# Kernel optimization log

Hardware: AMD Instinct MI355X
Metric: run time of the kernel (lower is better)

## Reference

```python
import math
import jax, jax.numpy as jnp
import numpy as np

B, N, C, H = 8, 512, 1024, 16
HD = C // H


def setup_inputs() -> dict:
    key = jax.random.key(0)
    ks = jax.random.split(key, 10)
    s = 0.02
    return {
        "x": jax.random.normal(ks[0], (B, N, C), jnp.float32),
        "mu": jax.random.normal(ks[1], (B, N, C), jnp.float32),
        "logvar": jax.random.normal(ks[2], (B, N, C), jnp.float32) * 0.1,
        "alpha": jax.random.uniform(ks[3], (B, N, 1), jnp.float32, 0.05, 1.0),
        "pi": jax.random.uniform(ks[4], (B, N, 1), jnp.float32, 0.05, 1.0),
        "z": jax.random.normal(ks[5], (B, N, C), jnp.float32),
        "w_q": jax.random.normal(ks[6], (C, C), jnp.float32) * s,
        "w_k": jax.random.normal(ks[7], (C, C), jnp.float32) * s,
        "w_v": jax.random.normal(ks[8], (C, C), jnp.float32) * s,
        "w_p": jax.random.normal(ks[9], (C, C), jnp.float32) * s,
        "b_p": jnp.zeros((C,), jnp.float32),
    }


def reference(x, mu, logvar, alpha, pi, z, w_q, w_k, w_v, w_p, b_p):
    # Non-meta NVIB path (set_mata_training_mode=False, qkv_bias=False).
    sqrt_hd = math.sqrt(HD)
    q = x @ w_q.T                                   # (B,N,C)
    biased_var = jnp.exp(logvar) + sqrt_hd          # (B,Nl,C)
    k = (mu / biased_var) @ w_k.T                   # (B,Nl,C)
    v = (sqrt_hd / biased_var * mu) @ w_v.T         # (B,Nl,C)

    def split_heads(t):
        b, n, _ = t.shape
        return t.reshape(b, n, H, HD).transpose(0, 2, 1, 3)  # (B,H,n,HD)

    qh, kh, vh = split_heads(q), split_heads(k), split_heads(v)
    attn = jnp.einsum("bhnd,bhmd->bhnm", qh, kh)    # (B,H,N,Nl)
    # additive log-alpha minus L2-norm bias, broadcast over heads and queries
    l2 = 0.5 * jnp.sum((mu / jnp.sqrt(biased_var)) ** 2, axis=-1)  # (B,Nl)
    bias = jnp.log(alpha[..., 0]) - l2              # (B,Nl)
    attn = attn + bias[:, None, None, :]
    attn = jax.nn.softmax(attn, axis=-1)
    out = jnp.einsum("bhnm,bhmd->bhnd", attn, vh)   # (B,H,N,HD)
    out = out.transpose(0, 2, 1, 3).reshape(x.shape[0], x.shape[1], C)
    out = out @ w_p.T + b_p
    return (out, attn)
```

## Files before the change

### kernel.cpp

```cpp
#include <hip/hip_runtime.h>
#include <hip/hip_bf16.h>

#define B_  8
#define N_  512
#define C_  1024
#define H_  16
#define HD_ 64
#define M_  4096

typedef float  f32x4  __attribute__((ext_vector_type(4)));
typedef __bf16 bf16x8 __attribute__((ext_vector_type(8)));
typedef unsigned short ushort_t;

__device__ __forceinline__ ushort_t f2bf(float f) {
  union { float f; unsigned int u; } un; un.f = f;
  unsigned int u = un.u;
  return (ushort_t)((u + 0x7fffu + ((u >> 16) & 1u)) >> 16);
}

__device__ __forceinline__ void gload16(const void* g, void* l) {
  __builtin_amdgcn_global_load_lds((const __attribute__((address_space(1))) void*)g,
                                   (__attribute__((address_space(3))) void*)l, 16, 0, 0);
}
#define SBAR()  __builtin_amdgcn_s_barrier()
#define SCHED() __builtin_amdgcn_sched_barrier(0)
#define VMCNT4() asm volatile("s_waitcnt vmcnt(4)" ::: "memory")
#define VMCNT0() asm volatile("s_waitcnt vmcnt(0)" ::: "memory")

__global__ __launch_bounds__(256) void prep_kernel(
    const float* __restrict__ x, const float* __restrict__ mu,
    const float* __restrict__ logvar, const float* __restrict__ alpha,
    const float* __restrict__ wq, const float* __restrict__ wk,
    const float* __restrict__ wv, const float* __restrict__ wp,
    ushort_t* __restrict__ xb, ushort_t* __restrict__ kp, ushort_t* __restrict__ vp,
    float* __restrict__ biasv, ushort_t* __restrict__ wb) {
  const int t = threadIdx.x;
  if (blockIdx.x >= 4096) {
    int i = ((blockIdx.x - 4096) * 256 + t) * 4;
    int sel = i >> 20;
    int off = i & 0xFFFFF;
    const float* src = sel == 0 ? wq : sel == 1 ? wk : sel == 2 ? wv : wp;
    float4 v = *(const float4*)(src + off);
    ushort4 o;
    o.x = f2bf(v.x); o.y = f2bf(v.y); o.z = f2bf(v.z); o.w = f2bf(v.w);
    *(ushort4*)(wb + i) = o;
    return;
  }
  const int row = blockIdx.x;
  const int base = row * C_ + t * 4;
  float4 xv = *(const float4*)(x + base);
  float4 mv = *(const float4*)(mu + base);
  float4 lv = *(const float4*)(logvar + base);
  float xa[4] = {xv.x, xv.y, xv.z, xv.w};
  float ma[4] = {mv.x, mv.y, mv.z, mv.w};
  float la[4] = {lv.x, lv.y, lv.z, lv.w};
  ushort4 xs, ks, vs;
  ushort_t* xsp = &xs.x; ushort_t* ksp = &ks.x; ushort_t* vsp = &vs.x;
  float l2 = 0.f;
#pragma unroll
  for (int i = 0; i < 4; ++i) {
    float bv  = __expf(la[i]) + 8.0f;
    float inv = 1.0f / bv;
    float kf  = ma[i] * inv;
    float vf  = 8.0f * ma[i] * inv;
    l2 += ma[i] * ma[i] * inv;
    xsp[i] = f2bf(xa[i]); ksp[i] = f2bf(kf); vsp[i] = f2bf(vf);
  }
  *(ushort4*)(xb + base) = xs;
  *(ushort4*)(kp + base) = ks;
  *(ushort4*)(vp + base) = vs;
  l2 += __shfl_xor(l2, 1);  l2 += __shfl_xor(l2, 2);  l2 += __shfl_xor(l2, 4);
  l2 += __shfl_xor(l2, 8);  l2 += __shfl_xor(l2, 16); l2 += __shfl_xor(l2, 32);
  __shared__ float red[4];
  if ((t & 63) == 0) red[t >> 6] = l2;
  __syncthreads();
  if (t == 0) {
    float s = red[0] + red[1] + red[2] + red[3];
    biasv[row] = __logf(alpha[row]) - 0.5f * s;
  }
}

__device__ __forceinline__ void gemm_tile_r3(const ushort_t* __restrict__ Ag,
                                             const ushort_t* __restrict__ Wg,
                                             int m0, int n0, f32x4 acc[4][4],
                                             ushort_t* lds) {
  const int t = threadIdx.x;
  const int w = t >> 6, lane = t & 63;
  const int wm = w >> 1, wn = w & 1;
  const int chunk = lane >> 4, r15 = lane & 15;
  const int s0 = t, s1 = t + 256;

#define RSTAGE(kt, buf)                                                           \
  do {                                                                            \
    const int k0 = (kt) * 32;                                                     \
    gload16(Ag + (size_t)(m0 + (s0 & 127)) * 1024 + k0 + (s0 >> 7) * 8,           \
            lds + (buf) * 4096 + (s0 & ~63) * 8);                                 \
    gload16(Ag + (size_t)(m0 + (s1 & 127)) * 1024 + k0 + (s1 >> 7) * 8,           \
            lds + (buf) * 4096 + (s1 & ~63) * 8);                                 \
    gload16(Wg + (size_t)(n0 + (s0 & 127)) * 1024 + k0 + (s0 >> 7) * 8,           \
            lds + 12288 + (buf) * 4096 + (s0 & ~63) * 8);                         \
    gload16(Wg + (size_t)(n0 + (s1 & 127)) * 1024 + k0 + (s1 >> 7) * 8,           \
            lds + 12288 + (buf) * 4096 + (s1 & ~63) * 8);                         \
  } while (0)

#define RCOMPUTE(j)                                                               \
  do {                                                                            \
    const ushort_t* Ab = lds + (j) * 4096;                                        \
    const ushort_t* Bb = lds + 12288 + (j) * 4096;                                \
    bf16x8 af[4], bw[4];                                                          \
    _Pragma("unroll")                                                             \
    for (int mi = 0; mi < 4; ++mi)                                                \
      af[mi] = *(const bf16x8*)(Ab + (chunk * 128 + wm * 64 + mi * 16 + r15) * 8);\
    _Pragma("unroll")                                                             \
    for (int ni = 0; ni < 4; ++ni)                                                \
      bw[ni] = *(const bf16x8*)(Bb + (chunk * 128 + wn * 64 + ni * 16 + r15) * 8);\
    __builtin_amdgcn_s_setprio(1);                                                \
    _Pragma("unroll")                                                             \
    for (int mi = 0; mi < 4; ++mi)                                                \
      _Pragma("unroll")                                                           \
      for (int ni = 0; ni < 4; ++ni)                                              \
        acc[mi][ni] = __builtin_amdgcn_mfma_f32_16x16x32_bf16(af[mi], bw[ni],     \
                                                              acc[mi][ni], 0, 0, 0); \
    __builtin_amdgcn_s_setprio(0);                                                \
    SCHED();                                                                      \
  } while (0)

  RSTAGE(0, 0); RSTAGE(1, 1);
  VMCNT4();
  SBAR(); SCHED();
  for (int kt0 = 0; kt0 < 30; kt0 += 3) {
    RSTAGE(kt0 + 2, 2); RCOMPUTE(0); VMCNT4(); SBAR(); SCHED();
    RSTAGE(kt0 + 3, 0); RCOMPUTE(1); VMCNT4(); SBAR(); SCHED();
    RSTAGE(kt0 + 4, 1); RCOMPUTE(2); VMCNT4(); SBAR(); SCHED();
  }
  RCOMPUTE(0); VMCNT0(); SBAR(); SCHED();
  RCOMPUTE(1);
#undef RSTAGE
#undef RCOMPUTE
}

__global__ __launch_bounds__(256, 3) void gemm_qkv_kernel(
    const ushort_t* __restrict__ xb, const ushort_t* __restrict__ kp,
    const ushort_t* __restrict__ vp, const ushort_t* __restrict__ wb,
    ushort_t* __restrict__ Qg, ushort_t* __restrict__ Kg, ushort_t* __restrict__ Vt) {
  __shared__ ushort_t lds[24576];
  const int z = blockIdx.z;
  const ushort_t* Ag = z == 0 ? xb : z == 1 ? kp : vp;
  const ushort_t* Wg = wb + (size_t)z * 1048576;
  const int m0 = blockIdx.x * 128, n0 = blockIdx.y * 128;
  f32x4 acc[4][4] = {};
  gemm_tile_r3(Ag, Wg, m0, n0, acc, lds);
  const int t = threadIdx.x, w = t >> 6, lane = t & 63;
  const int wm = w >> 1, wn = w & 1;
  const int hi = lane >> 4, r15 = lane & 15;

  __syncthreads();
  if (z < 2) {
    ushort_t* T = lds;
#pragma unroll
    for (int mi = 0; mi < 4; ++mi)
#pragma unroll
      for (int ni = 0; ni < 4; ++ni)
#pragma unroll
        for (int q = 0; q < 4; ++q) {
          int row = wm * 64 + mi * 16 + hi * 4 + q;
          int col = wn * 64 + ni * 16 + r15;
          T[row * 136 + col] = f2bf(acc[mi][ni][q]);
        }
    __syncthreads();
    ushort_t* Out = z == 0 ? Qg : Kg;
#pragma unroll
    for (int i = 0; i < 8; ++i) {
      int c = t + 256 * i;
      int row = c >> 4, col0 = (c & 15) * 8;
      bf16x8 v = *(const bf16x8*)(T + row * 136 + col0);
      *(bf16x8*)(Out + (size_t)(m0 + row) * 1024 + n0 + col0) = v;
    }
  } else {
    ushort_t* T = lds;
#pragma unroll
    for (int mi = 0; mi < 4; ++mi)
#pragma unroll
      for (int ni = 0; ni < 4; ++ni)
#pragma unroll
        for (int q = 0; q < 4; ++q) {
          int row = wm * 64 + mi * 16 + hi * 4 + q;
          int col = wn * 64 + ni * 16 + r15;
          T[row * 129 + col] = f2bf(acc[mi][ni][q]);
        }
    __syncthreads();
    const int b  = m0 >> 9;
    const int pb = m0 & 511;
#pragma unroll
    for (int i = 0; i < 8; ++i) {
      int c = t + 256 * i;
      int pc = c & 15, dl = c >> 4;
      bf16x8 v;
#pragma unroll
      for (int j = 0; j < 8; ++j)
        v[j] = *(const __bf16*)(T + (pc * 8 + j) * 129 + dl);
      int n = n0 + dl;
      int h = n >> 6, d = n & 63;
      *(bf16x8*)(Vt + (size_t)((b * 16 + h) * 64 + d) * 512 + pb + pc * 8) = v;
    }
  }
}

__global__ __launch_bounds__(256, 2) void attn_kernel(
    const ushort_t* __restrict__ Qg, const ushort_t* __restrict__ Kg,
    const ushort_t* __restrict__ Vt, const float* __restrict__ biasv,
    float* __restrict__ attn_out, ushort_t* __restrict__ Og) {
  __shared__ ushort_t Qt[4096];
  __shared__ ushort_t KV[16384];
  __shared__ ushort_t Pl[8192];
  __shared__ float biasl[512];
  const int bh = blockIdx.x, qt = blockIdx.y;
  const int b = bh >> 4, h = bh & 15;
  const int t = threadIdx.x, w = t >> 6, lane = t & 63;
  const int hi = lane >> 4, r15 = lane & 15;

  {
    float2 bv2 = *(const float2*)(biasv + b * 512 + t * 2);
    biasl[t * 2] = bv2.x; biasl[t * 2 + 1] = bv2.y;
  }
  {
    int s0 = t, s1 = t + 256;
    gload16(Qg + (size_t)(b * 512 + qt * 64 + (s0 & 63)) * 1024 + h * 64 + (s0 >> 6) * 8,
            Qt + (s0 & ~63) * 8);
    gload16(Qg + (size_t)(b * 512 + qt * 64 + (s1 & 63)) * 1024 + h * 64 + (s1 >> 6) * 8,
            Qt + (s1 & ~63) * 8);
  }

#define STAGE_K(kt, buf)                                                               \
  do {                                                                                 \
    _Pragma("unroll")                                                                  \
    for (int r = 0; r < 4; ++r) {                                                      \
      int s = r * 256 + t;                          \
      gload16(Kg + (size_t)(b * 512 + (kt) * 128 + (s & 127)) * 1024 + h * 64 + (s >> 7) * 8, \
              KV + (buf) * 8192 + (s & ~63) * 8);                                      \
    }                                                                                  \
  } while (0)
#define STAGE_V(kt, buf)                                                               \
  do {                                                                                 \
    _Pragma("unroll")                                                                  \
    for (int r = 0; r < 4; ++r) {                                                      \
      int s = r * 256 + t;                             \
      gload16(Vt + (size_t)(bh * 64 + (s & 63)) * 512 + (kt) * 128 + (s >> 6) * 8,     \
              KV + (buf) * 8192 + (s & ~63) * 8);                                      \
    }                                                                                  \
  } while (0)

  STAGE_K(0, 0);
  f32x4 acc[32] = {};
  bf16x8 aq[2];
  int cur = 0;

#pragma unroll
  for (int kt = 0; kt < 4; ++kt) {
    if (kt < 3) STAGE_K(kt + 1, cur ^ 1);
    else        STAGE_V(0, cur ^ 1);
    VMCNT4();
    SBAR();
    SCHED();
    if (kt == 0) {
#pragma unroll
      for (int ks = 0; ks < 2; ++ks)
        aq[ks] = *(const bf16x8*)(Qt + ((ks * 4 + hi) * 64 + w * 16 + r15) * 8);
    }
    __builtin_amdgcn_s_setprio(1);
#pragma unroll
    for (int mf = 0; mf < 8; ++mf)
#pragma unroll
      for (int ks = 0; ks < 2; ++ks) {
        bf16x8 bk = *(const bf16x8*)(KV + cur * 8192 + ((ks * 4 + hi) * 128 + mf * 16 + r15) * 8);
        acc[kt * 8 + mf] = __builtin_amdgcn_mfma_f32_16x16x32_bf16(aq[ks], bk, acc[kt * 8 + mf], 0, 0, 0);
      }
    __builtin_amdgcn_s_setprio(0);
    SCHED();
    SBAR();
    SCHED();
    cur ^= 1;
  }

  float mx[4] = {-1e30f, -1e30f, -1e30f, -1e30f};
#pragma unroll
  for (int f = 0; f < 32; ++f) {
    float bv = biasl[f * 16 + r15];
#pragma unroll
    for (int q = 0; q < 4; ++q) {
      acc[f][q] += bv;
      mx[q] = fmaxf(mx[q], acc[f][q]);
    }
  }
#pragma unroll
  for (int q = 0; q < 4; ++q) {
    mx[q] = fmaxf(mx[q], __shfl_xor(mx[q], 1));
    mx[q] = fmaxf(mx[q], __shfl_xor(mx[q], 2));
    mx[q] = fmaxf(mx[q], __shfl_xor(mx[q], 4));
    mx[q] = fmaxf(mx[q], __shfl_xor(mx[q], 8));
  }
  float sm[4] = {0.f, 0.f, 0.f, 0.f};
#pragma unroll
  for (int f = 0; f < 32; ++f)
#pragma unroll
    for (int q = 0; q < 4; ++q) {
      float p = __expf(acc[f][q] - mx[q]);
      acc[f][q] = p;
      sm[q] += p;
    }
#pragma unroll
  for (int q = 0; q < 4; ++q) {
    sm[q] += __shfl_xor(sm[q], 1);
    sm[q] += __shfl_xor(sm[q], 2);
    sm[q] += __shfl_xor(sm[q], 4);
    sm[q] += __shfl_xor(sm[q], 8);
    sm[q] = 1.0f / sm[q];
  }
#pragma unroll
  for (int f = 0; f < 32; ++f)
#pragma unroll
    for (int q = 0; q < 4; ++q)
      acc[f][q] *= sm[q];

  f32x4 oacc[4] = {};
#pragma unroll
  for (int kt = 0; kt < 4; ++kt) {
    if (kt < 3) STAGE_V(kt + 1, cur ^ 1);
#pragma unroll
    for (int fl = 0; fl < 8; ++fl) {
      int f = kt * 8 + fl;
      int chunkp = fl * 2 + (r15 >> 3);
#pragma unroll
      for (int q = 0; q < 4; ++q)
        Pl[w * 2048 + (chunkp * 16 + hi * 4 + q) * 8 + (lane & 7)] = f2bf(acc[f][q]);
    }
    if (kt < 3) VMCNT4(); else VMCNT0();
    SBAR();
    SCHED();
    __builtin_amdgcn_s_setprio(1);
#pragma unroll
    for (int ks = 0; ks < 4; ++ks) {
      bf16x8 pa = *(const bf16x8*)(Pl + w * 2048 + ((ks * 4 + hi) * 16 + r15) * 8);
#pragma unroll
      for (int df = 0; df < 4; ++df) {
        bf16x8 vb = *(const bf16x8*)(KV + cur * 8192 + ((ks * 4 + hi) * 64 + df * 16 + r15) * 8);
        oacc[df] = __builtin_amdgcn_mfma_f32_16x16x32_bf16(pa, vb, oacc[df], 0, 0, 0);
      }
    }
    __builtin_amdgcn_s_setprio(0);
    SCHED();
    SBAR();
    SCHED();
    cur ^= 1;
  }

  float* ao = attn_out + ((size_t)bh * 512 + qt * 64 + w * 16 + hi * 4) * 512 + r15;
#pragma unroll
  for (int f = 0; f < 32; ++f)
#pragma unroll
    for (int q = 0; q < 4; ++q)
      ao[(size_t)q * 512 + f * 16] = acc[f][q];

  size_t obase = (size_t)(b * 512 + qt * 64 + w * 16 + hi * 4) * 1024 + h * 64 + r15;
#pragma unroll
  for (int df = 0; df < 4; ++df)
#pragma unroll
    for (int q = 0; q < 4; ++q)
      Og[obase + (size_t)q * 1024 + df * 16] = f2bf(oacc[df][q]);
#undef STAGE_K
#undef STAGE_V
}

__global__ __launch_bounds__(256, 3) void gemm_out_kernel(
    const ushort_t* __restrict__ Og, const ushort_t* __restrict__ wb,
    const float* __restrict__ bp, float* __restrict__ out) {
  __shared__ ushort_t lds[24576];
  const int m0 = blockIdx.x * 128, n0 = blockIdx.y * 128;
  f32x4 acc[4][4] = {};
  gemm_tile_r3(Og, wb + 3 * 1048576, m0, n0, acc, lds);
  const int t = threadIdx.x, w = t >> 6, lane = t & 63;
  const int wm = w >> 1, wn = w & 1;
  const int rbase = m0 + wm * 64 + (lane >> 4) * 4;
  const int cbase = n0 + wn * 64 + (lane & 15);
#pragma unroll
  for (int mi = 0; mi < 4; ++mi)
#pragma unroll
    for (int ni = 0; ni < 4; ++ni) {
      float bias = bp[cbase + ni * 16];
#pragma unroll
      for (int q = 0; q < 4; ++q)
        out[(size_t)(rbase + mi * 16 + q) * 1024 + cbase + ni * 16] = acc[mi][ni][q] + bias;
    }
}

extern "C" void kernel_launch(void* const* d_in, const int* in_sizes, int n_in,
                              void* d_out, int out_size, void* d_ws, size_t ws_size,
                              hipStream_t stream) {
  const float* x      = (const float*)d_in[0];
  const float* mu     = (const float*)d_in[1];
  const float* logvar = (const float*)d_in[2];
  const float* alpha  = (const float*)d_in[3];
  const float* wq = (const float*)d_in[6];
  const float* wk = (const float*)d_in[7];
  const float* wv = (const float*)d_in[8];
  const float* wp = (const float*)d_in[9];
  const float* bp = (const float*)d_in[10];

  float* out      = (float*)d_out;
  float* attn_out = out + (size_t)M_ * C_;

  char* ws = (char*)d_ws;
  ushort_t* xb    = (ushort_t*)(ws);
  ushort_t* kp    = (ushort_t*)(ws + (size_t)8  * 1048576);
  ushort_t* vp    = (ushort_t*)(ws + (size_t)16 * 1048576);
  ushort_t* Qg    = (ushort_t*)(ws + (size_t)24 * 1048576);
  ushort_t* Kg    = (ushort_t*)(ws + (size_t)32 * 1048576);
  ushort_t* Vt    = (ushort_t*)(ws + (size_t)40 * 1048576);
  ushort_t* wb    = (ushort_t*)(ws + (size_t)48 * 1048576);
  float*    biasv = (float*)   (ws + (size_t)56 * 1048576);
  ushort_t* Og    = xb;

  prep_kernel<<<8192, 256, 0, stream>>>(x, mu, logvar, alpha, wq, wk, wv, wp,
                                        xb, kp, vp, biasv, wb);
  gemm_qkv_kernel<<<dim3(32, 8, 3), 256, 0, stream>>>(xb, kp, vp, wb, Qg, Kg, Vt);
  attn_kernel<<<dim3(128, 8), 256, 0, stream>>>(Qg, Kg, Vt, biasv, attn_out, Og);
  gemm_out_kernel<<<dim3(32, 8), 256, 0, stream>>>(Og, wb, bp, out);
}
```

Measured before the change: 135.9 us.

## Store intermediates in pre-tiled layouts so every tile load is contiguous

Intermediate bf16 buffers (inputs, weights, Q/K/V, attention output) are now written in tile-blocked layouts that match the LDS staging order of each consumer kernel. Every global-to-LDS load then reads one contiguous 8KB/16KB block instead of strided 16-byte pieces spread over rows. The aim is to improve DRAM and cache-line efficiency for the GEMM and attention loads. In exchange the producer stores become scattered, and the index math is more complex and must match across all four kernels.

```diff
diff --git a/kernel.cpp b/kernel.cpp
--- a/kernel.cpp
+++ b/kernel.cpp
@@ -26,6 +26,7 @@
 #define SCHED() __builtin_amdgcn_sched_barrier(0)
 #define VMCNT4() asm volatile("s_waitcnt vmcnt(4)" ::: "memory")
 #define VMCNT0() asm volatile("s_waitcnt vmcnt(0)" ::: "memory")
+
 
 __global__ __launch_bounds__(256) void prep_kernel(
     const float* __restrict__ x, const float* __restrict__ mu,
@@ -43,7 +44,10 @@
     float4 v = *(const float4*)(src + off);
     ushort4 o;
     o.x = f2bf(v.x); o.y = f2bf(v.y); o.z = f2bf(v.z); o.w = f2bf(v.w);
-    *(ushort4*)(wb + i) = o;
+    int n = off >> 10, k4 = off & 1023;
+    size_t po = ((size_t)((n >> 7) * 32 + (k4 >> 5)) * 4 + ((k4 >> 3) & 3)) * 1024
+              + (n & 127) * 8 + (k4 & 7);
+    *(ushort4*)(wb + sel * 1048576 + po) = o;
     return;
   }
   const int row = blockIdx.x;
@@ -66,9 +70,13 @@
     l2 += ma[i] * ma[i] * inv;
     xsp[i] = f2bf(xa[i]); ksp[i] = f2bf(kf); vsp[i] = f2bf(vf);
   }
-  *(ushort4*)(xb + base) = xs;
-  *(ushort4*)(kp + base) = ks;
-  *(ushort4*)(vp + base) = vs;
+  {
+    size_t po = ((size_t)((row >> 7) * 32 + (t >> 3)) * 4 + ((t >> 1) & 3)) * 1024
+              + (row & 127) * 8 + (t & 1) * 4;
+    *(ushort4*)(xb + po) = xs;
+    *(ushort4*)(kp + po) = ks;
+    *(ushort4*)(vp + po) = vs;
+  }
   l2 += __shfl_xor(l2, 1);  l2 += __shfl_xor(l2, 2);  l2 += __shfl_xor(l2, 4);
   l2 += __shfl_xor(l2, 8);  l2 += __shfl_xor(l2, 16); l2 += __shfl_xor(l2, 32);
   __shared__ float red[4];
@@ -82,7 +90,7 @@
 
 __device__ __forceinline__ void gemm_tile_r3(const ushort_t* __restrict__ Ag,
                                              const ushort_t* __restrict__ Wg,
-                                             int m0, int n0, f32x4 acc[4][4],
+                                             int amt, int ant, f32x4 acc[4][4],
                                              ushort_t* lds) {
   const int t = threadIdx.x;
   const int w = t >> 6, lane = t & 63;
@@ -92,15 +100,12 @@
 
 #define RSTAGE(kt, buf)                                                           \
   do {                                                                            \
-    const int k0 = (kt) * 32;                                                     \
-    gload16(Ag + (size_t)(m0 + (s0 & 127)) * 1024 + k0 + (s0 >> 7) * 8,           \
-            lds + (buf) * 4096 + (s0 & ~63) * 8);                                 \
-    gload16(Ag + (size_t)(m0 + (s1 & 127)) * 1024 + k0 + (s1 >> 7) * 8,           \
-            lds + (buf) * 4096 + (s1 & ~63) * 8);                                 \
-    gload16(Wg + (size_t)(n0 + (s0 & 127)) * 1024 + k0 + (s0 >> 7) * 8,           \
-            lds + 12288 + (buf) * 4096 + (s0 & ~63) * 8);                         \
-    gload16(Wg + (size_t)(n0 + (s1 & 127)) * 1024 + k0 + (s1 >> 7) * 8,           \
-            lds + 12288 + (buf) * 4096 + (s1 & ~63) * 8);                         \
+    const ushort_t* sa = Ag + (size_t)(amt * 32 + (kt)) * 4096;                   \
+    const ushort_t* sb = Wg + (size_t)(ant * 32 + (kt)) * 4096;                   \
+    gload16(sa + s0 * 8, lds + (buf) * 4096 + (s0 & ~63) * 8);                    \
+    gload16(sa + s1 * 8, lds + (buf) * 4096 + (s1 & ~63) * 8);                    \
+    gload16(sb + s0 * 8, lds + 12288 + (buf) * 4096 + (s0 & ~63) * 8);            \
+    gload16(sb + s1 * 8, lds + 12288 + (buf) * 4096 + (s1 & ~63) * 8);            \
   } while (0)
 
 #define RCOMPUTE(j)                                                               \
@@ -142,17 +147,18 @@
 __global__ __launch_bounds__(256, 3) void gemm_qkv_kernel(
     const ushort_t* __restrict__ xb, const ushort_t* __restrict__ kp,
     const ushort_t* __restrict__ vp, const ushort_t* __restrict__ wb,
-    ushort_t* __restrict__ Qg, ushort_t* __restrict__ Kg, ushort_t* __restrict__ Vt) {
+    ushort_t* __restrict__ Qhs, ushort_t* __restrict__ Khs, ushort_t* __restrict__ Vts) {
   __shared__ ushort_t lds[24576];
   const int z = blockIdx.z;
   const ushort_t* Ag = z == 0 ? xb : z == 1 ? kp : vp;
   const ushort_t* Wg = wb + (size_t)z * 1048576;
   const int m0 = blockIdx.x * 128, n0 = blockIdx.y * 128;
   f32x4 acc[4][4] = {};
-  gemm_tile_r3(Ag, Wg, m0, n0, acc, lds);
+  gemm_tile_r3(Ag, Wg, blockIdx.x, blockIdx.y, acc, lds);
   const int t = threadIdx.x, w = t >> 6, lane = t & 63;
   const int wm = w >> 1, wn = w & 1;
   const int hi = lane >> 4, r15 = lane & 15;
+  const int b = m0 >> 9, h0 = n0 >> 6;
 
   __syncthreads();
   if (z < 2) {
@@ -168,13 +174,26 @@
           T[row * 136 + col] = f2bf(acc[mi][ni][q]);
         }
     __syncthreads();
-    ushort_t* Out = z == 0 ? Qg : Kg;
-#pragma unroll
-    for (int i = 0; i < 8; ++i) {
-      int c = t + 256 * i;
-      int row = c >> 4, col0 = (c & 15) * 8;
-      bf16x8 v = *(const bf16x8*)(T + row * 136 + col0);
-      *(bf16x8*)(Out + (size_t)(m0 + row) * 1024 + n0 + col0) = v;
+    if (z == 0) {
+      const int qt0 = (m0 & 511) >> 6;
+#pragma unroll
+      for (int i = 0; i < 8; ++i) {
+        int c = t + 256 * i;
+        int row64 = c & 63, qt_l = (c >> 6) & 1, chunk = (c >> 7) & 7, head_l = (c >> 10) & 1;
+        bf16x8 v = *(const bf16x8*)(T + (qt_l * 64 + row64) * 136 + head_l * 64 + chunk * 8);
+        int bh = b * 16 + h0 + head_l;
+        *(bf16x8*)(Qhs + ((size_t)((bh * 8 + qt0 + qt_l) * 8 + chunk) * 64 + row64) * 8) = v;
+      }
+    } else {
+      const int kt = (m0 & 511) >> 7;
+#pragma unroll
+      for (int i = 0; i < 8; ++i) {
+        int c = t + 256 * i;
+        int row128 = c & 127, chunk = (c >> 7) & 7, head_l = (c >> 10) & 1;
+        bf16x8 v = *(const bf16x8*)(T + row128 * 136 + head_l * 64 + chunk * 8);
+        int bh = b * 16 + h0 + head_l;
+        *(bf16x8*)(Khs + ((size_t)((bh * 4 + kt) * 8 + chunk) * 128 + row128) * 8) = v;
+      }
     }
   } else {
     ushort_t* T = lds;
@@ -189,26 +208,24 @@
           T[row * 129 + col] = f2bf(acc[mi][ni][q]);
         }
     __syncthreads();
-    const int b  = m0 >> 9;
-    const int pb = m0 & 511;
+    const int kt = (m0 & 511) >> 7;
 #pragma unroll
     for (int i = 0; i < 8; ++i) {
       int c = t + 256 * i;
-      int pc = c & 15, dl = c >> 4;
+      int d64 = c & 63, head_l = (c >> 6) & 1, chunkp = (c >> 7) & 15;
       bf16x8 v;
 #pragma unroll
       for (int j = 0; j < 8; ++j)
-        v[j] = *(const __bf16*)(T + (pc * 8 + j) * 129 + dl);
-      int n = n0 + dl;
-      int h = n >> 6, d = n & 63;
-      *(bf16x8*)(Vt + (size_t)((b * 16 + h) * 64 + d) * 512 + pb + pc * 8) = v;
+        v[j] = *(const __bf16*)(T + (chunkp * 8 + j) * 129 + head_l * 64 + d64);
+      int bh = b * 16 + h0 + head_l;
+      *(bf16x8*)(Vts + ((size_t)((bh * 4 + kt) * 16 + chunkp) * 64 + d64) * 8) = v;
     }
   }
 }
 
 __global__ __launch_bounds__(256, 2) void attn_kernel(
-    const ushort_t* __restrict__ Qg, const ushort_t* __restrict__ Kg,
-    const ushort_t* __restrict__ Vt, const float* __restrict__ biasv,
+    const ushort_t* __restrict__ Qhs, const ushort_t* __restrict__ Khs,
+    const ushort_t* __restrict__ Vts, const float* __restrict__ biasv,
     float* __restrict__ attn_out, ushort_t* __restrict__ Og) {
   __shared__ ushort_t Qt[4096];
   __shared__ ushort_t KV[16384];
@@ -224,29 +241,27 @@
     biasl[t * 2] = bv2.x; biasl[t * 2 + 1] = bv2.y;
   }
   {
-    int s0 = t, s1 = t + 256;
-    gload16(Qg + (size_t)(b * 512 + qt * 64 + (s0 & 63)) * 1024 + h * 64 + (s0 >> 6) * 8,
-            Qt + (s0 & ~63) * 8);
-    gload16(Qg + (size_t)(b * 512 + qt * 64 + (s1 & 63)) * 1024 + h * 64 + (s1 >> 6) * 8,
-            Qt + (s1 & ~63) * 8);
+    const ushort_t* sq = Qhs + (size_t)(bh * 8 + qt) * 4096;
+    gload16(sq + t * 8, Qt + (t & ~63) * 8);
+    gload16(sq + (t + 256) * 8, Qt + ((t + 256) & ~63) * 8);
   }
 
 #define STAGE_K(kt, buf)                                                               \
   do {                                                                                 \
+    const ushort_t* sk = Khs + (size_t)(bh * 4 + (kt)) * 8192;                         \
     _Pragma("unroll")                                                                  \
     for (int r = 0; r < 4; ++r) {                                                      \
-      int s = r * 256 + t;                          \
-      gload16(Kg + (size_t)(b * 512 + (kt) * 128 + (s & 127)) * 1024 + h * 64 + (s >> 7) * 8, \
-              KV + (buf) * 8192 + (s & ~63) * 8);                                      \
+      int s = r * 256 + t;                                                             \
+      gload16(sk + s * 8, KV + (buf) * 8192 + (s & ~63) * 8);                          \
     }                                                                                  \
   } while (0)
 #define STAGE_V(kt, buf)                                                               \
   do {                                                                                 \
+    const ushort_t* sv = Vts + (size_t)(bh * 4 + (kt)) * 8192;                         \
     _Pragma("unroll")                                                                  \
     for (int r = 0; r < 4; ++r) {                                                      \
-      int s = r * 256 + t;                             \
-      gload16(Vt + (size_t)(bh * 64 + (s & 63)) * 512 + (kt) * 128 + (s >> 6) * 8,     \
-              KV + (buf) * 8192 + (s & ~63) * 8);                                      \
+      int s = r * 256 + t;                                                             \
+      gload16(sv + s * 8, KV + (buf) * 8192 + (s & ~63) * 8);                          \
     }                                                                                  \
   } while (0)
 
@@ -361,12 +376,19 @@
     for (int q = 0; q < 4; ++q)
       ao[(size_t)q * 512 + f * 16] = acc[f][q];
 
-  size_t obase = (size_t)(b * 512 + qt * 64 + w * 16 + hi * 4) * 1024 + h * 64 + r15;
-#pragma unroll
-  for (int df = 0; df < 4; ++df)
-#pragma unroll
-    for (int q = 0; q < 4; ++q)
-      Og[obase + (size_t)q * 1024 + df * 16] = f2bf(oacc[df][q]);
+  {
+    const int mtile = b * 4 + (qt >> 1);
+    const int rowl = (qt & 1) * 64 + w * 16 + hi * 4;
+#pragma unroll
+    for (int df = 0; df < 4; ++df) {
+      int kto = h * 2 + (df >> 1);
+      int chunko = (df & 1) * 2 + (r15 >> 3);
+      size_t ob = ((size_t)((mtile * 32 + kto) * 4 + chunko) * 1024 + (r15 & 7));
+#pragma unroll
+      for (int q = 0; q < 4; ++q)
+        Og[ob + (size_t)(rowl + q) * 8] = f2bf(oacc[df][q]);
+    }
+  }
 #undef STAGE_K
 #undef STAGE_V
 }
@@ -377,7 +399,7 @@
   __shared__ ushort_t lds[24576];
   const int m0 = blockIdx.x * 128, n0 = blockIdx.y * 128;
   f32x4 acc[4][4] = {};
-  gemm_tile_r3(Og, wb + 3 * 1048576, m0, n0, acc, lds);
+  gemm_tile_r3(Og, wb + 3 * 1048576, blockIdx.x, blockIdx.y, acc, lds);
   const int t = threadIdx.x, w = t >> 6, lane = t & 63;
   const int wm = w >> 1, wn = w & 1;
   const int rbase = m0 + wm * 64 + (lane >> 4) * 4;
@@ -413,16 +435,16 @@
   ushort_t* xb    = (ushort_t*)(ws);
   ushort_t* kp    = (ushort_t*)(ws + (size_t)8  * 1048576);
   ushort_t* vp    = (ushort_t*)(ws + (size_t)16 * 1048576);
-  ushort_t* Qg    = (ushort_t*)(ws + (size_t)24 * 1048576);
-  ushort_t* Kg    = (ushort_t*)(ws + (size_t)32 * 1048576);
-  ushort_t* Vt    = (ushort_t*)(ws + (size_t)40 * 1048576);
+  ushort_t* Qhs   = (ushort_t*)(ws + (size_t)24 * 1048576);
+  ushort_t* Khs   = (ushort_t*)(ws + (size_t)32 * 1048576);
+  ushort_t* Vts   = (ushort_t*)(ws + (size_t)40 * 1048576);
   ushort_t* wb    = (ushort_t*)(ws + (size_t)48 * 1048576);
   float*    biasv = (float*)   (ws + (size_t)56 * 1048576);
   ushort_t* Og    = xb;
 
   prep_kernel<<<8192, 256, 0, stream>>>(x, mu, logvar, alpha, wq, wk, wv, wp,
                                         xb, kp, vp, biasv, wb);
-  gemm_qkv_kernel<<<dim3(32, 8, 3), 256, 0, stream>>>(xb, kp, vp, wb, Qg, Kg, Vt);
-  attn_kernel<<<dim3(128, 8), 256, 0, stream>>>(Qg, Kg, Vt, biasv, attn_out, Og);
+  gemm_qkv_kernel<<<dim3(32, 8, 3), 256, 0, stream>>>(xb, kp, vp, wb, Qhs, Khs, Vts);
+  attn_kernel<<<dim3(128, 8), 256, 0, stream>>>(Qhs, Khs, Vts, biasv, attn_out, Og);
   gemm_out_kernel<<<dim3(32, 8), 256, 0, stream>>>(Og, wb, bp, out);
 }
```

New measurement: 130.3 us. -4.1%, faster.
